# Kernel optimization log

Hardware: AMD Instinct MI355X
Metric: run time of the kernel (lower is better)

## Reference

```python
import jax, jax.numpy as jnp
import numpy as np

N = 8192   # nodes
F = 128    # features
ORDER = 4  # polynomial taps


def setup_inputs() -> dict:
    key = jax.random.key(0)
    k1, k2, k3 = jax.random.split(key, 3)
    X = jax.random.normal(k1, (N, F), dtype=jnp.float32)
    # scale GSO so powers don't blow up (spectral-norm-ish normalization)
    S = jax.random.normal(k2, (N, N), dtype=jnp.float32) / jnp.sqrt(jnp.float32(N))
    coefficients = jax.random.uniform(k3, (ORDER,), dtype=jnp.float32)
    return {"X": X, "S": S, "coefficients": coefficients}


def reference(X, S, coefficients):
    # y = sum_{k=0}^{K-1} h_k * S^k X
    Z = X
    y = coefficients[0] * Z
    for k in range(1, ORDER):  # small fixed tap count; loop over taps, not data
        Z = S @ Z              # S^k X, [N, F]
        y = y + coefficients[k] * Z
    return y
```

## Files before the change

kernel.cpp:

```cpp
#include <hip/hip_runtime.h>
#include <hip/hip_bf16.h>
#include <stdint.h>


typedef __attribute__((ext_vector_type(8))) short     bf16x8;
typedef __attribute__((ext_vector_type(8))) uint16_t  u16x8;
typedef __attribute__((ext_vector_type(4))) uint16_t  u16x4;
typedef __attribute__((ext_vector_type(4))) float     f32x4;

#define NN 8192
#define NF 128
#define ZSTRIDE (8192 + 64)

#define WAITV(n) asm volatile("s_waitcnt vmcnt(" #n ")" ::: "memory")
#define WAITL0   asm volatile("s_waitcnt lgkmcnt(0)" ::: "memory")

__device__ inline uint16_t f2bf(float f) {
    uint32_t u = __builtin_bit_cast(uint32_t, f);
    u += 0x7fffu + ((u >> 16) & 1u);
    return (uint16_t)(u >> 16);
}

__device__ inline void gl2lds16(const void* g, uint8_t* l) {
    __builtin_amdgcn_global_load_lds(
        (const __attribute__((address_space(1))) uint32_t*)g,
        (__attribute__((address_space(3))) uint32_t*)l,
        16, 0, 0);
}

__device__ inline bf16x8 ld16(const uint8_t* p) {
    return __builtin_bit_cast(bf16x8, *(const u16x8*)p);
}

__global__ __launch_bounds__(256) void k_prep(const float* __restrict__ X,
                                              const float* __restrict__ coeff,
                                              float* __restrict__ y,
                                              uint16_t* __restrict__ ZT0) {
    __shared__ float tile[16][NF + 4];
    const int t  = threadIdx.x;
    const int r0 = blockIdx.x * 16;
    const float h0 = coeff[0];
#pragma unroll
    for (int i = 0; i < 2; ++i) {
        int o   = (i * 256 + t) * 4;
        int row = o >> 7, col = o & 127;
        f32x4 v = *(const f32x4*)(X + (size_t)(r0 + row) * NF + col);
        *(f32x4*)&tile[row][col] = v;
        *(f32x4*)(y + (size_t)(r0 + row) * NF + col) = v * h0;
    }
    __syncthreads();
    const int c = t >> 1, rh = t & 1;
    u16x8 pk;
#pragma unroll
    for (int e = 0; e < 8; ++e) pk[e] = f2bf(tile[rh * 8 + e][c]);
    *(u16x8*)(ZT0 + (size_t)c * ZSTRIDE + r0 + rh * 8) = pk;
}

template<int KS>
__global__ __launch_bounds__(512, 4) void k_gemm_bf(
    const uint16_t* __restrict__ S16, const uint16_t* __restrict__ ZTin,
    float* __restrict__ P)
{
    __shared__ __align__(16) uint8_t smem[2][24576];
    const int t = threadIdx.x, lane = t & 63;
    const int w = t >> 6, m = lane & 15, g = lane >> 4;
    const int rt = w & 3, ch = w >> 2;
    const int mt = blockIdx.x & 127, ks = blockIdx.x >> 7;
    const int r0 = mt * 64;
    const int kb = ks * (NN / KS);
    constexpr int NT = (NN / KS) / 64;

    const int srow = t >> 3, sc = t & 7;
    const int scs  = (sc ^ (srow & 7)) << 3;
    const uint16_t* asrc = S16  + (size_t)(r0 + srow) * NN + kb + scs;
    const uint16_t* bsrc = ZTin + (size_t)srow * ZSTRIDE   + kb + scs;

    const int sw   = m & 7;
    const int aoff = (rt * 16 + m) * 128 + ((g ^ sw) << 4);
    const int bof  = 8192 + (ch * 64 + m) * 128 + ((g ^ sw) << 4);

    f32x4 acc[4] = {};

    {
        uint8_t* b = smem[0];
        gl2lds16(asrc, b + t * 16);
        gl2lds16(bsrc, b + 8192 + t * 16);
        gl2lds16(bsrc + (size_t)64 * ZSTRIDE, b + 16384 + t * 16);
    }
    int cur = 0;
#pragma unroll 1
    for (int kt = 0; kt < NT; ++kt) {
        if (kt + 1 < NT) {
            const int ko = (kt + 1) * 64;
            uint8_t* b = smem[cur ^ 1];
            gl2lds16(asrc + ko, b + t * 16);
            gl2lds16(bsrc + ko, b + 8192 + t * 16);
            gl2lds16(bsrc + (size_t)64 * ZSTRIDE + ko, b + 16384 + t * 16);
            WAITV(3);
        } else {
            WAITV(0);
        }
        __builtin_amdgcn_s_barrier();
        __builtin_amdgcn_sched_barrier(0);
        const uint8_t* bb = smem[cur];
        bf16x8 a0 = ld16(bb + aoff);
        bf16x8 a1 = ld16(bb + (aoff ^ 64));
#pragma unroll
        for (int ct = 0; ct < 4; ++ct) {
            acc[ct] = __builtin_amdgcn_mfma_f32_16x16x32_bf16(
                a0, ld16(bb + bof + ct * 16 * 128), acc[ct], 0, 0, 0);
            acc[ct] = __builtin_amdgcn_mfma_f32_16x16x32_bf16(
                a1, ld16(bb + ((bof + ct * 16 * 128) ^ 64)), acc[ct], 0, 0, 0);
        }
        WAITL0;
        __builtin_amdgcn_sched_barrier(0);
        __builtin_amdgcn_s_barrier();
        cur ^= 1;
    }

    float* pb = P + ((size_t)ks * NN + r0 + rt * 16 + 4 * g) * NF + ch * 64 + m;
#pragma unroll
    for (int ct = 0; ct < 4; ++ct)
#pragma unroll
        for (int i = 0; i < 4; ++i)
            pb[(size_t)i * NF + ct * 16] = acc[ct][i];
}

template<int KS>
__global__ __launch_bounds__(512, 4) void k_gemm_cv(
    const float* __restrict__ Sf, const uint16_t* __restrict__ ZTin,
    float* __restrict__ P, uint16_t* __restrict__ S16)
{
    __shared__ __align__(16) uint8_t smem[2][32768];
    const int t = threadIdx.x, lane = t & 63;
    const int w = t >> 6, m = lane & 15, g = lane >> 4;
    const int rt = w & 3, ch = w >> 2;
    const int mt = blockIdx.x & 127, ks = blockIdx.x >> 7;
    const int r0 = mt * 64;
    const int kb = ks * (NN / KS);
    constexpr int NT = (NN / KS) / 64;

    const int arow = t >> 4, ac = t & 15;
    const int acg  = ac ^ ((arow & 7) << 1);
    const float* asrc = Sf + (size_t)(r0 + arow) * NN + kb + (acg << 2);
    const int brow = t >> 3, bc = t & 7;
    const uint16_t* bsrc = ZTin + (size_t)brow * ZSTRIDE + kb
                           + ((bc ^ (brow & 7)) << 3);

    const int sw  = m & 7;
    const int ab  = (rt * 16 + m) * 256 + (((g * 2) ^ (sw << 1)) << 4);
    const int bof = 16384 + (ch * 64 + m) * 128 + ((g ^ sw) << 4);

    uint16_t* s16o = S16 + (size_t)(r0 + arow) * NN + kb + (acg << 2);

    f32x4 acc[4] = {};

    {
        uint8_t* b = smem[0];
        gl2lds16(asrc, b + t * 16);
        gl2lds16(asrc + (size_t)32 * NN, b + 8192 + t * 16);
        gl2lds16(bsrc, b + 16384 + t * 16);
        gl2lds16(bsrc + (size_t)64 * ZSTRIDE, b + 24576 + t * 16);
    }
    int cur = 0;
#pragma unroll 1
    for (int kt = 0; kt < NT; ++kt) {
        if (kt + 1 < NT) {
            const int ko = (kt + 1) * 64;
            uint8_t* b = smem[cur ^ 1];
            gl2lds16(asrc + ko, b + t * 16);
            gl2lds16(asrc + (size_t)32 * NN + ko, b + 8192 + t * 16);
            gl2lds16(bsrc + ko, b + 16384 + t * 16);
            gl2lds16(bsrc + (size_t)64 * ZSTRIDE + ko, b + 24576 + t * 16);
            WAITV(4);
        } else {
            WAITV(0);
        }
        __builtin_amdgcn_s_barrier();
        __builtin_amdgcn_sched_barrier(0);
        const uint8_t* bb = smem[cur];

        bf16x8 a0, a1;
        {
            f32x4 lo = *(const f32x4*)(bb + ab);
            f32x4 hi = *(const f32x4*)(bb + ab + 16);
            u16x8 p;
#pragma unroll
            for (int j = 0; j < 4; ++j) { p[j] = f2bf(lo[j]); p[j + 4] = f2bf(hi[j]); }
            a0 = __builtin_bit_cast(bf16x8, p);
            lo = *(const f32x4*)(bb + (ab ^ 128));
            hi = *(const f32x4*)(bb + (ab ^ 128) + 16);
#pragma unroll
            for (int j = 0; j < 4; ++j) { p[j] = f2bf(lo[j]); p[j + 4] = f2bf(hi[j]); }
            a1 = __builtin_bit_cast(bf16x8, p);
        }
#pragma unroll
        for (int ct = 0; ct < 4; ++ct) {
            acc[ct] = __builtin_amdgcn_mfma_f32_16x16x32_bf16(
                a0, ld16(bb + bof + ct * 16 * 128), acc[ct], 0, 0, 0);
            acc[ct] = __builtin_amdgcn_mfma_f32_16x16x32_bf16(
                a1, ld16(bb + ((bof + ct * 16 * 128) ^ 64)), acc[ct], 0, 0, 0);
        }
#pragma unroll
        for (int h = 0; h < 2; ++h) {
            f32x4 v = *(const f32x4*)(bb + h * 8192 + t * 16);
            u16x4 s;
#pragma unroll
            for (int j = 0; j < 4; ++j) s[j] = f2bf(v[j]);
            *(u16x4*)(s16o + (size_t)h * 32 * NN + kt * 64) = s;
        }
        WAITL0;
        __builtin_amdgcn_sched_barrier(0);
        __builtin_amdgcn_s_barrier();
        cur ^= 1;
    }

    float* pb = P + ((size_t)ks * NN + r0 + rt * 16 + 4 * g) * NF + ch * 64 + m;
#pragma unroll
    for (int ct = 0; ct < 4; ++ct)
#pragma unroll
        for (int i = 0; i < 4; ++i)
            pb[(size_t)i * NF + ct * 16] = acc[ct][i];
}

template<int KS, bool WRITE_ZT>
__global__ __launch_bounds__(256) void k_combine(const float* __restrict__ P,
                                                 float* __restrict__ y,
                                                 uint16_t* __restrict__ ZTout,
                                                 const float* __restrict__ coeff,
                                                 int pass) {
    __shared__ float tile[16][NF + 4];
    const int t = threadIdx.x, r0 = blockIdx.x * 16;
    const float hk = coeff[pass];
    const int row = t >> 4, col = (t & 15) * 8;
    const size_t off = (size_t)(r0 + row) * NF + col;
    f32x4 s0 = *(const f32x4*)(P + off);
    f32x4 s1 = *(const f32x4*)(P + off + 4);
#pragma unroll
    for (int k = 1; k < KS; ++k) {
        s0 += *(const f32x4*)(P + (size_t)k * NN * NF + off);
        s1 += *(const f32x4*)(P + (size_t)k * NN * NF + off + 4);
    }
    float* yp = y + off;
    f32x4 y0 = *(const f32x4*)yp, y1 = *(const f32x4*)(yp + 4);
    *(f32x4*)yp       = y0 + hk * s0;
    *(f32x4*)(yp + 4) = y1 + hk * s1;
    if (WRITE_ZT) {
        *(f32x4*)&tile[row][col]     = s0;
        *(f32x4*)&tile[row][col + 4] = s1;
        __syncthreads();
        const int c = t >> 1, rh = t & 1;
        u16x8 pk;
#pragma unroll
        for (int e = 0; e < 8; ++e) pk[e] = f2bf(tile[rh * 8 + e][c]);
        *(u16x8*)(ZTout + (size_t)c * ZSTRIDE + r0 + rh * 8) = pk;
    }
}

template<int KS>
static void run(const float* X, const float* S, const float* coeff, float* y,
                uint16_t* ZT0, uint16_t* ZT1, uint16_t* S16, float* P,
                hipStream_t stream) {
    k_prep<<<dim3(512), dim3(256), 0, stream>>>(X, coeff, y, ZT0);
    k_gemm_cv<KS><<<dim3(128 * KS), dim3(512), 0, stream>>>(S, ZT0, P, S16);
    k_combine<KS, true ><<<dim3(512), dim3(256), 0, stream>>>(P, y, ZT1, coeff, 1);
    k_gemm_bf<KS><<<dim3(128 * KS), dim3(512), 0, stream>>>(S16, ZT1, P);
    k_combine<KS, true ><<<dim3(512), dim3(256), 0, stream>>>(P, y, ZT0, coeff, 2);
    k_gemm_bf<KS><<<dim3(128 * KS), dim3(512), 0, stream>>>(S16, ZT0, P);
    k_combine<KS, false><<<dim3(512), dim3(256), 0, stream>>>(P, y, nullptr, coeff, 3);
}

extern "C" void kernel_launch(void* const* d_in, const int* in_sizes, int n_in,
                              void* d_out, int out_size, void* d_ws, size_t ws_size,
                              hipStream_t stream) {
    const float* X     = (const float*)d_in[0];
    const float* S     = (const float*)d_in[1];
    const float* coeff = (const float*)d_in[2];
    float* y = (float*)d_out;

    uint8_t* ws = (uint8_t*)d_ws;
    const size_t zb     = ((size_t)NF * ZSTRIDE * sizeof(uint16_t) + 255) & ~(size_t)255;
    const size_t s16b   = (size_t)NN * NN * sizeof(uint16_t);
    const size_t base   = 2 * zb + s16b;
    const size_t pslice = (size_t)NN * NF * sizeof(float);
    uint16_t* ZT0 = (uint16_t*)ws;
    uint16_t* ZT1 = (uint16_t*)(ws + zb);
    uint16_t* S16 = (uint16_t*)(ws + 2 * zb);
    float*    P   = (float*)(ws + base);

    if (ws_size >= base + 4 * pslice)
        run<4>(X, S, coeff, y, ZT0, ZT1, S16, P, stream);
    else if (ws_size >= base + 2 * pslice)
        run<2>(X, S, coeff, y, ZT0, ZT1, S16, P, stream);
    else
        run<1>(X, S, coeff, y, ZT0, ZT1, S16, P, stream);
}
```

Before: 211.1 us.

## Split S fp32-to-bf16 conversion into standalone kernel; triple-buffer bf16 GEMM pipeline

Removes the fused convert-and-multiply first-pass GEMM and replaces it with a dedicated grid-stride streaming kernel that converts S to bf16 using nontemporal loads, followed by the regular bf16 GEMM. The bf16 GEMM now uses three LDS buffers with a two-tile-deep prefetch instead of double buffering, to hide more global-load latency. The trade-off is an extra full pass over S16 (a write then a read of 128MB of bf16) in place of the fused path, plus higher LDS use per block, which may reduce occupancy.

```diff
diff --git a/kernel.cpp b/kernel.cpp
--- a/kernel.cpp
+++ b/kernel.cpp
@@ -5,7 +5,6 @@
 
 typedef __attribute__((ext_vector_type(8))) short     bf16x8;
 typedef __attribute__((ext_vector_type(8))) uint16_t  u16x8;
-typedef __attribute__((ext_vector_type(4))) uint16_t  u16x4;
 typedef __attribute__((ext_vector_type(4))) float     f32x4;
 
 #define NN 8192
@@ -30,6 +29,20 @@
 
 __device__ inline bf16x8 ld16(const uint8_t* p) {
     return __builtin_bit_cast(bf16x8, *(const u16x8*)p);
+}
+
+__global__ __launch_bounds__(256) void k_convert(const float* __restrict__ S,
+                                                 uint16_t* __restrict__ S16) {
+    const size_t n8 = (size_t)NN * NN / 8;
+    const size_t stride = (size_t)gridDim.x * 256;
+    for (size_t i = (size_t)blockIdx.x * 256 + threadIdx.x; i < n8; i += stride) {
+        f32x4 a = __builtin_nontemporal_load((const f32x4*)(S + i * 8));
+        f32x4 b = __builtin_nontemporal_load((const f32x4*)(S + i * 8 + 4));
+        u16x8 p;
+#pragma unroll
+        for (int j = 0; j < 4; ++j) { p[j] = f2bf(a[j]); p[j + 4] = f2bf(b[j]); }
+        *(u16x8*)(S16 + i * 8) = p;
+    }
 }
 
 __global__ __launch_bounds__(256) void k_prep(const float* __restrict__ X,
@@ -61,7 +74,7 @@
     const uint16_t* __restrict__ S16, const uint16_t* __restrict__ ZTin,
     float* __restrict__ P)
 {
-    __shared__ __align__(16) uint8_t smem[2][24576];
+    __shared__ __align__(16) uint8_t smem[3][24576];
     const int t = threadIdx.x, lane = t & 63;
     const int w = t >> 6, m = lane & 15, g = lane >> 4;
     const int rt = w & 3, ch = w >> 2;
@@ -81,21 +94,24 @@
 
     f32x4 acc[4] = {};
 
-    {
-        uint8_t* b = smem[0];
-        gl2lds16(asrc, b + t * 16);
-        gl2lds16(bsrc, b + 8192 + t * 16);
-        gl2lds16(bsrc + (size_t)64 * ZSTRIDE, b + 16384 + t * 16);
-    }
+    auto stage = [&](int buf, int kt) {
+        const int ko = kt * 64;
+        uint8_t* b = smem[buf];
+        gl2lds16(asrc + ko, b + t * 16);
+        gl2lds16(bsrc + ko, b + 8192 + t * 16);
+        gl2lds16(bsrc + (size_t)64 * ZSTRIDE + ko, b + 16384 + t * 16);
+    };
+
+    stage(0, 0);
+    stage(1, 1);
     int cur = 0;
 #pragma unroll 1
     for (int kt = 0; kt < NT; ++kt) {
-        if (kt + 1 < NT) {
-            const int ko = (kt + 1) * 64;
-            uint8_t* b = smem[cur ^ 1];
-            gl2lds16(asrc + ko, b + t * 16);
-            gl2lds16(bsrc + ko, b + 8192 + t * 16);
-            gl2lds16(bsrc + (size_t)64 * ZSTRIDE + ko, b + 16384 + t * 16);
+        if (kt + 2 < NT) {
+            int nxt = cur + 2; if (nxt >= 3) nxt -= 3;
+            stage(nxt, kt + 2);
+            WAITV(6);
+        } else if (kt + 2 == NT) {
             WAITV(3);
         } else {
             WAITV(0);
@@ -115,104 +131,7 @@
         WAITL0;
         __builtin_amdgcn_sched_barrier(0);
         __builtin_amdgcn_s_barrier();
-        cur ^= 1;
-    }
-
-    float* pb = P + ((size_t)ks * NN + r0 + rt * 16 + 4 * g) * NF + ch * 64 + m;
-#pragma unroll
-    for (int ct = 0; ct < 4; ++ct)
-#pragma unroll
-        for (int i = 0; i < 4; ++i)
-            pb[(size_t)i * NF + ct * 16] = acc[ct][i];
-}
-
-template<int KS>
-__global__ __launch_bounds__(512, 4) void k_gemm_cv(
-    const float* __restrict__ Sf, const uint16_t* __restrict__ ZTin,
-    float* __restrict__ P, uint16_t* __restrict__ S16)
-{
-    __shared__ __align__(16) uint8_t smem[2][32768];
-    const int t = threadIdx.x, lane = t & 63;
-    const int w = t >> 6, m = lane & 15, g = lane >> 4;
-    const int rt = w & 3, ch = w >> 2;
-    const int mt = blockIdx.x & 127, ks = blockIdx.x >> 7;
-    const int r0 = mt * 64;
-    const int kb = ks * (NN / KS);
-    constexpr int NT = (NN / KS) / 64;
-
-    const int arow = t >> 4, ac = t & 15;
-    const int acg  = ac ^ ((arow & 7) << 1);
-    const float* asrc = Sf + (size_t)(r0 + arow) * NN + kb + (acg << 2);
-    const int brow = t >> 3, bc = t & 7;
-    const uint16_t* bsrc = ZTin + (size_t)brow * ZSTRIDE + kb
-                           + ((bc ^ (brow & 7)) << 3);
-
-    const int sw  = m & 7;
-    const int ab  = (rt * 16 + m) * 256 + (((g * 2) ^ (sw << 1)) << 4);
-    const int bof = 16384 + (ch * 64 + m) * 128 + ((g ^ sw) << 4);
-
-    uint16_t* s16o = S16 + (size_t)(r0 + arow) * NN + kb + (acg << 2);
-
-    f32x4 acc[4] = {};
-
-    {
-        uint8_t* b = smem[0];
-        gl2lds16(asrc, b + t * 16);
-        gl2lds16(asrc + (size_t)32 * NN, b + 8192 + t * 16);
-        gl2lds16(bsrc, b + 16384 + t * 16);
-        gl2lds16(bsrc + (size_t)64 * ZSTRIDE, b + 24576 + t * 16);
-    }
-    int cur = 0;
-#pragma unroll 1
-    for (int kt = 0; kt < NT; ++kt) {
-        if (kt + 1 < NT) {
-            const int ko = (kt + 1) * 64;
-            uint8_t* b = smem[cur ^ 1];
-            gl2lds16(asrc + ko, b + t * 16);
-            gl2lds16(asrc + (size_t)32 * NN + ko, b + 8192 + t * 16);
-            gl2lds16(bsrc + ko, b + 16384 + t * 16);
-            gl2lds16(bsrc + (size_t)64 * ZSTRIDE + ko, b + 24576 + t * 16);
-            WAITV(4);
-        } else {
-            WAITV(0);
-        }
-        __builtin_amdgcn_s_barrier();
-        __builtin_amdgcn_sched_barrier(0);
-        const uint8_t* bb = smem[cur];
-
-        bf16x8 a0, a1;
-        {
-            f32x4 lo = *(const f32x4*)(bb + ab);
-            f32x4 hi = *(const f32x4*)(bb + ab + 16);
-            u16x8 p;
-#pragma unroll
-            for (int j = 0; j < 4; ++j) { p[j] = f2bf(lo[j]); p[j + 4] = f2bf(hi[j]); }
-            a0 = __builtin_bit_cast(bf16x8, p);
-            lo = *(const f32x4*)(bb + (ab ^ 128));
-            hi = *(const f32x4*)(bb + (ab ^ 128) + 16);
-#pragma unroll
-            for (int j = 0; j < 4; ++j) { p[j] = f2bf(lo[j]); p[j + 4] = f2bf(hi[j]); }
-            a1 = __builtin_bit_cast(bf16x8, p);
-        }
-#pragma unroll
-        for (int ct = 0; ct < 4; ++ct) {
-            acc[ct] = __builtin_amdgcn_mfma_f32_16x16x32_bf16(
-                a0, ld16(bb + bof + ct * 16 * 128), acc[ct], 0, 0, 0);
-            acc[ct] = __builtin_amdgcn_mfma_f32_16x16x32_bf16(
-                a1, ld16(bb + ((bof + ct * 16 * 128) ^ 64)), acc[ct], 0, 0, 0);
-        }
-#pragma unroll
-        for (int h = 0; h < 2; ++h) {
-            f32x4 v = *(const f32x4*)(bb + h * 8192 + t * 16);
-            u16x4 s;
-#pragma unroll
-            for (int j = 0; j < 4; ++j) s[j] = f2bf(v[j]);
-            *(u16x4*)(s16o + (size_t)h * 32 * NN + kt * 64) = s;
-        }
-        WAITL0;
-        __builtin_amdgcn_sched_barrier(0);
-        __builtin_amdgcn_s_barrier();
-        cur ^= 1;
+        cur = (cur + 1 == 3) ? 0 : cur + 1;
     }
 
     float* pb = P + ((size_t)ks * NN + r0 + rt * 16 + 4 * g) * NF + ch * 64 + m;
@@ -262,7 +181,8 @@
                 uint16_t* ZT0, uint16_t* ZT1, uint16_t* S16, float* P,
                 hipStream_t stream) {
     k_prep<<<dim3(512), dim3(256), 0, stream>>>(X, coeff, y, ZT0);
-    k_gemm_cv<KS><<<dim3(128 * KS), dim3(512), 0, stream>>>(S, ZT0, P, S16);
+    k_convert<<<dim3(2048), dim3(256), 0, stream>>>(S, S16);
+    k_gemm_bf<KS><<<dim3(128 * KS), dim3(512), 0, stream>>>(S16, ZT0, P);
     k_combine<KS, true ><<<dim3(512), dim3(256), 0, stream>>>(P, y, ZT1, coeff, 1);
     k_gemm_bf<KS><<<dim3(128 * KS), dim3(512), 0, stream>>>(S16, ZT1, P);
     k_combine<KS, true ><<<dim3(512), dim3(256), 0, stream>>>(P, y, ZT0, coeff, 2);
```

After: 187.0 us. -11.4%, faster.
